# Performance work log

Hardware: AMD Instinct MI355X
Metric: run time of the kernel (lower is better)

Reference implementation:

```python
import jax, jax.numpy as jnp
import numpy as np

ALPHA = 0.2          # LeakyReLU negative slope
NEG = -9.0e15        # masking value from the torch code
B, N, F, O, H = 8, 1024, 256, 128, 8


def setup_inputs() -> dict:
    key = jax.random.key(0)
    ks = jax.random.split(key, 12)
    inputs = jax.random.normal(ks[0], (B, N, F), dtype=jnp.float32)
    adj = jax.random.randint(ks[1], (B, N, N), 0, 2, dtype=jnp.int32)
    mask = jnp.ones((B, N), dtype=jnp.float32)  # unused by forward, kept for signature fidelity
    s = 0.08
    # per-head GAT layers (stacked): W [H,F,O], attention vector a split into src/dst halves
    W_att = jax.random.normal(ks[2], (H, F, O), dtype=jnp.float32) * s
    a_src = jax.random.normal(ks[3], (H, O), dtype=jnp.float32) * s
    a_dst = jax.random.normal(ks[4], (H, O), dtype=jnp.float32) * s
    # output GAT layer: in = H*O, out = O
    W_out = jax.random.normal(ks[5], (H * O, O), dtype=jnp.float32) * s
    ao_src = jax.random.normal(ks[6], (O,), dtype=jnp.float32) * s
    ao_dst = jax.random.normal(ks[7], (O,), dtype=jnp.float32) * s
    # nn.Linear(H*O, O) and nn.Linear(O, O)
    lin_w = jax.random.normal(ks[8], (O, H * O), dtype=jnp.float32) * s
    lin_b = jax.random.normal(ks[9], (O,), dtype=jnp.float32) * s
    ln_w = jax.random.normal(ks[10], (O, O), dtype=jnp.float32) * s
    ln_b = jax.random.normal(ks[11], (O,), dtype=jnp.float32) * s
    return {"inputs": inputs, "adj": adj, "mask": mask, "W_att": W_att, "a_src": a_src,
            "a_dst": a_dst, "W_out": W_out, "ao_src": ao_src, "ao_dst": ao_dst,
            "lin_w": lin_w, "lin_b": lin_b, "ln_w": ln_w, "ln_b": ln_b}


def _gat_heads(x, adj, W, asrc, adst):
    # x: [B,N,Fin], W: [Hh,Fin,O]. e[b,h,i,j] = leakyrelu(h_i.a_src + h_j.a_dst)
    # (equal to torch's repeat/cat @ a without the O(N^2*2F) intermediate)
    h = jnp.einsum('bnf,hfo->bhno', x, W)
    s1 = jnp.einsum('bhno,ho->bhn', h, asrc)
    s2 = jnp.einsum('bhno,ho->bhn', h, adst)
    e = jax.nn.leaky_relu(s1[:, :, :, None] + s2[:, :, None, :], ALPHA)
    att = jax.nn.softmax(jnp.where(adj[:, None, :, :] > 0, e, NEG), axis=-1)
    return jnp.einsum('bhij,bhjo->bhio', att, h)  # [B,Hh,N,O]


def reference(inputs, adj, mask, W_att, a_src, a_dst, W_out, ao_src, ao_dst,
              lin_w, lin_b, ln_w, ln_b):
    b, n, _ = inputs.shape
    # layer 0: multi-head GAT, concat=True -> elu, then concat over heads
    hp = _gat_heads(inputs, adj, W_att, a_src, a_dst)              # [B,H,N,O]
    x = jax.nn.elu(hp).transpose(0, 2, 1, 3).reshape(b, n, -1)     # [B,N,H*O]
    # layer 1 (residual): linear(x) + out_att(x, adj) (concat=False, no elu)
    out = _gat_heads(x, adj, W_out[None], ao_src[None], ao_dst[None])[:, 0]  # [B,N,O]
    x = x @ lin_w.T + lin_b + out
    # final projection + relu
    return jax.nn.relu(x @ ln_w.T + ln_b)
```

## Files before the change

kernel.cpp:

```cpp
#include <hip/hip_runtime.h>


#define NN 1024
#define FF 256
#define OO 128
#define HH 8
#define HO 1024

typedef __attribute__((ext_vector_type(8))) short short8;
typedef __attribute__((ext_vector_type(4))) float floatx4;

__device__ __forceinline__ ushort f2b(float f) {
    union { float f; unsigned u; } v; v.f = f;
    unsigned r = v.u + 0x7FFFu + ((v.u >> 16) & 1u);
    return (ushort)(r >> 16);
}

__global__ __launch_bounds__(256) void pack_adj(
    const int* __restrict__ adj, unsigned long long* __restrict__ adjp)
{
    int w = blockIdx.x * 4 + (threadIdx.x >> 6);
    int lane = threadIdx.x & 63;
    const int* row = adj + (long)w * NN;
#pragma unroll
    for (int it = 0; it < 16; it++) {
        unsigned long long m = __ballot(row[it * 64 + lane] > 0);
        if (lane == 0) adjp[(long)w * 16 + it] = m;
    }
}

__global__ __launch_bounds__(256) void pack_weights(
    const float* __restrict__ W_att, const float* __restrict__ W_out,
    const float* __restrict__ lin_w, const float* __restrict__ ln_w,
    ushort* __restrict__ WAp, ushort* __restrict__ WOp,
    ushort* __restrict__ LWp, ushort* __restrict__ NWp)
{
    int tid = blockIdx.x * 256 + threadIdx.x;
    float v[8];
    ushort* dst;
    if (tid < 32768) {
        int h = tid >> 12, rem = tid & 4095, kc = rem >> 7, o = rem & 127;
        const float* s = W_att + h * 32768;
#pragma unroll
        for (int i = 0; i < 8; i++) v[i] = s[(kc * 8 + i) * 128 + o];
        dst = WAp + h * 32768 + kc * 1024 + o * 8;
    } else if (tid < 49152) {
        int t2 = tid - 32768;
        int kc = t2 >> 7, o = t2 & 127;
#pragma unroll
        for (int i = 0; i < 8; i++) v[i] = W_out[(kc * 8 + i) * 128 + o];
        dst = WOp + kc * 1024 + o * 8;
    } else if (tid < 65536) {
        int t3 = tid - 49152;
        int kc = t3 >> 7, c = t3 & 127;
        float4 a = *(const float4*)(lin_w + c * 1024 + kc * 8);
        float4 bq = *(const float4*)(lin_w + c * 1024 + kc * 8 + 4);
        v[0] = a.x; v[1] = a.y; v[2] = a.z; v[3] = a.w;
        v[4] = bq.x; v[5] = bq.y; v[6] = bq.z; v[7] = bq.w;
        dst = LWp + kc * 1024 + c * 8;
    } else {
        int t4 = tid - 65536;
        int kc = t4 >> 7, c = t4 & 127;
        float4 a = *(const float4*)(ln_w + c * 128 + kc * 8);
        float4 bq = *(const float4*)(ln_w + c * 128 + kc * 8 + 4);
        v[0] = a.x; v[1] = a.y; v[2] = a.z; v[3] = a.w;
        v[4] = bq.x; v[5] = bq.y; v[6] = bq.z; v[7] = bq.w;
        dst = NWp + kc * 1024 + c * 8;
    }
    union { ushort s[8]; uint4 q; } u;
#pragma unroll
    for (int i = 0; i < 8; i++) u.s[i] = f2b(v[i]);
    *(uint4*)dst = u.q;
}

__global__ __launch_bounds__(256) void gemmT0(
    const ushort* __restrict__ WAp, const float* __restrict__ inputs,
    ushort* __restrict__ Cb, float* __restrict__ s1, float* __restrict__ s2,
    const float* __restrict__ a1g, const float* __restrict__ a2g)
{
    __shared__ ushort Bs[32 * 520];
    int t = threadIdx.x;
    int wave = t >> 6, lane = t & 63;
    int quad = lane >> 4, l16 = lane & 15;
    int bh = blockIdx.y;
    int hh = bh & 7, b = bh >> 3;
    int nblk = blockIdx.x * 64;
    int n0w = nblk + wave * 16;

    const float* binp = inputs + ((long)b * NN + nblk) * FF;
#pragma unroll
    for (int it = 0; it < 8; it++) {
        int pid = it * 256 + t;
        int kc = pid & 31, r = pid >> 5;
        float4 va = *(const float4*)(binp + r * FF + kc * 8);
        float4 vb = *(const float4*)(binp + r * FF + kc * 8 + 4);
        union { ushort s[8]; uint4 q; } u;
        u.s[0] = f2b(va.x); u.s[1] = f2b(va.y); u.s[2] = f2b(va.z); u.s[3] = f2b(va.w);
        u.s[4] = f2b(vb.x); u.s[5] = f2b(vb.y); u.s[6] = f2b(vb.z); u.s[7] = f2b(vb.w);
        *(uint4*)&Bs[kc * 520 + r * 8] = u.q;
    }
    __syncthreads();

    const ushort* A = WAp + hh * 32768;
    int nl = wave * 16 + l16;
    floatx4 acc[8];
    floatx4 zero = {0.f, 0.f, 0.f, 0.f};
#pragma unroll
    for (int mt = 0; mt < 8; mt++) acc[mt] = zero;

#pragma unroll 2
    for (int kc2 = 0; kc2 < 8; kc2++) {
        int kc = kc2 * 4 + quad;
        short8 bfr = *(const short8*)&Bs[kc * 520 + nl * 8];
#pragma unroll
        for (int mt = 0; mt < 8; mt++) {
            short8 af = *(const short8*)(A + kc * 1024 + (mt * 16 + l16) * 8);
            acc[mt] = __builtin_amdgcn_mfma_f32_16x16x32_bf16(af, bfr, acc[mt], 0, 0, 0);
        }
    }

    const float* a1 = a1g + hh * OO;
    const float* a2 = a2g + hh * OO;
    float sp1 = 0.f, sp2 = 0.f;
#pragma unroll
    for (int mt = 0; mt < 8; mt++) {
        float4 v1 = *(const float4*)(a1 + mt * 16 + quad * 4);
        float4 v2 = *(const float4*)(a2 + mt * 16 + quad * 4);
        sp1 += acc[mt][0] * v1.x + acc[mt][1] * v1.y + acc[mt][2] * v1.z + acc[mt][3] * v1.w;
        sp2 += acc[mt][0] * v2.x + acc[mt][1] * v2.y + acc[mt][2] * v2.z + acc[mt][3] * v2.w;
    }
    sp1 += __shfl_xor(sp1, 16); sp1 += __shfl_xor(sp1, 32);
    sp2 += __shfl_xor(sp2, 16); sp2 += __shfl_xor(sp2, 32);
    if (lane < 16) {
        s1[(long)bh * NN + n0w + l16] = sp1;
        s2[(long)bh * NN + n0w + l16] = sp2;
    }

    ushort* cb = Cb + (long)bh * OO * NN;
    int n = n0w + l16;
    int base = (n >> 3) * 1024 + (n & 7);
#pragma unroll
    for (int mt = 0; mt < 8; mt++) {
#pragma unroll
        for (int reg = 0; reg < 4; reg++) {
            int o = mt * 16 + quad * 4 + reg;
            cb[base + o * 8] = f2b(acc[mt][reg]);
        }
    }
}

__global__ __launch_bounds__(256) void gemmT_sk(
    const ushort* __restrict__ WOp,
    const ushort* __restrict__ Bb,
    ushort* __restrict__ Cb,
    float* __restrict__ s1, float* __restrict__ s2,
    const float* __restrict__ a1g, const float* __restrict__ a2g)
{
    __shared__ float red[4 * 2304];
    int t = threadIdx.x;
    int wave = t >> 6, lane = t & 63;
    int quad = lane >> 4, l16 = lane & 15;
    int b = blockIdx.y;
    int n0 = blockIdx.x * 16;

    const ushort* brow = Bb + ((long)b * NN + n0 + l16) * HO;
    int kbase = wave * 256;

    floatx4 acc[8];
    floatx4 zero = {0.f, 0.f, 0.f, 0.f};
#pragma unroll
    for (int mt = 0; mt < 8; mt++) acc[mt] = zero;

    for (int k0 = 0; k0 < 256; k0 += 32) {
        int kb = kbase + k0 + quad * 8;
        int kch = kb >> 3;
        short8 bfr = *(const short8*)(brow + kb);
#pragma unroll
        for (int mt = 0; mt < 8; mt++) {
            short8 af = *(const short8*)(WOp + kch * 1024 + (mt * 16 + l16) * 8);
            acc[mt] = __builtin_amdgcn_mfma_f32_16x16x32_bf16(af, bfr, acc[mt], 0, 0, 0);
        }
    }

#pragma unroll
    for (int mt = 0; mt < 8; mt++)
#pragma unroll
        for (int reg = 0; reg < 4; reg++)
            red[wave * 2304 + (mt * 16 + quad * 4 + reg) * 18 + l16] = acc[mt][reg];
    __syncthreads();

    int nl = t & 15, g = t >> 4, o0 = g * 8;
    float s[8];
#pragma unroll
    for (int k = 0; k < 8; k++) {
        int idx = (o0 + k) * 18 + nl;
        s[k] = red[idx] + red[2304 + idx] + red[4608 + idx] + red[6912 + idx];
    }

    float p1 = 0.f, p2 = 0.f;
#pragma unroll
    for (int k = 0; k < 8; k++) {
        p1 += s[k] * a1g[o0 + k];
        p2 += s[k] * a2g[o0 + k];
    }

    ushort* cb = Cb + (long)b * OO * NN;
    int nglob = n0 + nl;
    int base = (nglob >> 3) * 1024 + (nglob & 7);
#pragma unroll
    for (int k = 0; k < 8; k++) cb[base + (o0 + k) * 8] = f2b(s[k]);

    __syncthreads();
    red[g * 16 + nl] = p1;
    red[256 + g * 16 + nl] = p2;
    __syncthreads();
    if (t < 16) {
        float q1 = 0.f, q2 = 0.f;
#pragma unroll
        for (int gg = 0; gg < 16; gg++) {
            q1 += red[gg * 16 + t];
            q2 += red[256 + gg * 16 + t];
        }
        s1[(long)b * NN + n0 + t] = q1;
        s2[(long)b * NN + n0 + t] = q2;
    }
}

template <int JS>
__global__ __launch_bounds__(256) void attn_mfma(
    const float* __restrict__ s1g, const float* __restrict__ s2g,
    const ushort* __restrict__ hTp, const uint* __restrict__ adjp,
    float* __restrict__ outf, ushort* __restrict__ outb,
    int Hh, int outStride, int doElu, int writeBf)
{
    extern __shared__ float smem_f[];
    float* s2s = smem_f;
    float* red = smem_f + NN;
    float* Lred = red + 8448;

    int t = threadIdx.x;
    int wave = t >> 6, lane = t & 63;
    int quad = lane >> 4, l16 = lane & 15;
    int bh = blockIdx.y;
    int hh = bh % Hh, b = bh / Hh;

    const float* s2r = s2g + (long)bh * NN;
    for (int j = t; j < NN; j += 256) s2s[j] = s2r[j];
    __syncthreads();

    const ushort* hT = hTp + (long)bh * OO * NN;
    const ushort* hbase = hT + quad * 1024 + l16 * 8;
    floatx4 zero = {0.f, 0.f, 0.f, 0.f};

    if (JS == 2) {
        int ig = wave >> 1, jh = wave & 1;
        int i0 = blockIdx.x * 64 + ig * 32;
        int j_lo = jh * (NN / 2), j_hi = j_lo + NN / 2;

        float s1a = s1g[(long)bh * NN + i0 + l16];
        float s1b = s1g[(long)bh * NN + i0 + 16 + l16];
        const uint* abA = adjp + ((long)b * NN + i0 + l16) * 32;
        const uint* abB = abA + 16 * 32;

        floatx4 acc0[8], acc1[8];
#pragma unroll
        for (int ot = 0; ot < 8; ot++) { acc0[ot] = zero; acc1[ot] = zero; }
        float Lp0 = 0.f, Lp1 = 0.f;

        for (int j0 = j_lo; j0 < j_hi; j0 += 32) {
            const ushort* hp = hbase + (j0 >> 3) * 1024;
            short8 bf[8];
#pragma unroll
            for (int ot = 0; ot < 8; ot++)
                bf[ot] = *(const short8*)(hp + ot * 128);
            uint mbA = (abA[j0 >> 5] >> (quad * 8)) & 0xffu;
            uint mbB = (abB[j0 >> 5] >> (quad * 8)) & 0xffu;
            int kb = j0 + quad * 8;
            float4 sA4 = *(const float4*)(s2s + kb);
            float4 sB4 = *(const float4*)(s2s + kb + 4);
            float se[8] = {sA4.x, sA4.y, sA4.z, sA4.w, sB4.x, sB4.y, sB4.z, sB4.w};
            short8 afA, afB;
#pragma unroll
            for (int e = 0; e < 8; e++) {
                float ea = s1a + se[e]; ea = fmaxf(ea, 0.2f * ea);
                float eb = s1b + se[e]; eb = fmaxf(eb, 0.2f * eb);
                union { float f; uint u; } wa, wb;
                wa.f = ((mbA >> e) & 1u) ? __expf(ea) : 0.f;
                wb.f = ((mbB >> e) & 1u) ? __expf(eb) : 0.f;
                wa.u &= 0xffff0000u; wb.u &= 0xffff0000u;
                afA[e] = (short)(wa.u >> 16);
                afB[e] = (short)(wb.u >> 16);
                Lp0 += wa.f; Lp1 += wb.f;
            }
#pragma unroll
            for (int ot = 0; ot < 8; ot++) {
                acc0[ot] = __builtin_amdgcn_mfma_f32_16x16x32_bf16(afA, bf[ot], acc0[ot], 0, 0, 0);
                acc1[ot] = __builtin_amdgcn_mfma_f32_16x16x32_bf16(afB, bf[ot], acc1[ot], 0, 0, 0);
            }
        }

        Lp0 += __shfl_xor(Lp0, 16); Lp0 += __shfl_xor(Lp0, 32);
        Lp1 += __shfl_xor(Lp1, 16); Lp1 += __shfl_xor(Lp1, 32);

        if (jh == 1) {
#pragma unroll
            for (int ot = 0; ot < 8; ot++)
#pragma unroll
                for (int reg = 0; reg < 4; reg++) {
                    red[(ig * 32 + quad * 4 + reg) * 132 + ot * 16 + l16] = acc0[ot][reg];
                    red[(ig * 32 + 16 + quad * 4 + reg) * 132 + ot * 16 + l16] = acc1[ot][reg];
                }
            if (lane < 16) {
                Lred[(ig * 2 + 0) * 16 + l16] = Lp0;
                Lred[(ig * 2 + 1) * 16 + l16] = Lp1;
            }
        }
        __syncthreads();
        if (jh == 0) {
            float r0 = 1.0f / (Lp0 + Lred[(ig * 2 + 0) * 16 + l16]);
            float r1 = 1.0f / (Lp1 + Lred[(ig * 2 + 1) * 16 + l16]);
#pragma unroll
            for (int tile = 0; tile < 2; tile++) {
                float rv = tile ? r1 : r0;
                floatx4* ac = tile ? acc1 : acc0;
#pragma unroll
                for (int reg = 0; reg < 4; reg++) {
                    float linv = __shfl(rv, quad * 4 + reg);
                    int rloc = ig * 32 + tile * 16 + quad * 4 + reg;
                    int row = blockIdx.x * 64 + rloc;
                    if (writeBf) {
                        ushort* orow = outb + (long)b * NN * outStride + hh * OO +
                                       (long)row * outStride + l16;
#pragma unroll
                        for (int ot = 0; ot < 8; ot++) {
                            float v = (ac[ot][reg] + red[rloc * 132 + ot * 16 + l16]) * linv;
                            if (doElu) v = (v > 0.f) ? v : (__expf(v) - 1.0f);
                            orow[ot * 16] = f2b(v);
                        }
                    } else {
                        float* orow = outf + (long)b * NN * outStride + hh * OO +
                                      (long)row * outStride + l16;
#pragma unroll
                        for (int ot = 0; ot < 8; ot++) {
                            float v = (ac[ot][reg] + red[rloc * 132 + ot * 16 + l16]) * linv;
                            if (doElu) v = (v > 0.f) ? v : (__expf(v) - 1.0f);
                            orow[ot * 16] = v;
                        }
                    }
                }
            }
        }
    } else {
        int i0 = blockIdx.x * 16;
        int j_lo = wave * (NN / 4), j_hi = j_lo + NN / 4;

        float s1a = s1g[(long)bh * NN + i0 + l16];
        const uint* abA = adjp + ((long)b * NN + i0 + l16) * 32;

        floatx4 acc[8];
#pragma unroll
        for (int ot = 0; ot < 8; ot++) acc[ot] = zero;
        float Lp = 0.f;

        for (int j0 = j_lo; j0 < j_hi; j0 += 32) {
            const ushort* hp = hbase + (j0 >> 3) * 1024;
            short8 bf[8];
#pragma unroll
            for (int ot = 0; ot < 8; ot++)
                bf[ot] = *(const short8*)(hp + ot * 128);
            uint mbA = (abA[j0 >> 5] >> (quad * 8)) & 0xffu;
            int kb = j0 + quad * 8;
            float4 sA4 = *(const float4*)(s2s + kb);
            float4 sB4 = *(const float4*)(s2s + kb + 4);
            float se[8] = {sA4.x, sA4.y, sA4.z, sA4.w, sB4.x, sB4.y, sB4.z, sB4.w};
            short8 afA;
#pragma unroll
            for (int e = 0; e < 8; e++) {
                float ea = s1a + se[e]; ea = fmaxf(ea, 0.2f * ea);
                union { float f; uint u; } wa;
                wa.f = ((mbA >> e) & 1u) ? __expf(ea) : 0.f;
                wa.u &= 0xffff0000u;
                afA[e] = (short)(wa.u >> 16);
                Lp += wa.f;
            }
#pragma unroll
            for (int ot = 0; ot < 8; ot++)
                acc[ot] = __builtin_amdgcn_mfma_f32_16x16x32_bf16(afA, bf[ot], acc[ot], 0, 0, 0);
        }

        Lp += __shfl_xor(Lp, 16); Lp += __shfl_xor(Lp, 32);
#pragma unroll
        for (int ot = 0; ot < 8; ot++)
#pragma unroll
            for (int reg = 0; reg < 4; reg++)
                red[(wave * 16 + quad * 4 + reg) * 132 + ot * 16 + l16] = acc[ot][reg];
        if (lane < 16) Lred[wave * 16 + l16] = Lp;
        __syncthreads();
        int row = t >> 4, c0 = (t & 15) * 8;
        float L = Lred[row] + Lred[16 + row] + Lred[32 + row] + Lred[48 + row];
        float rinv = 1.0f / L;
        int grow = i0 + row;
        float vv[8];
#pragma unroll
        for (int k = 0; k < 8; k++) {
            float s = red[row * 132 + c0 + k] + red[(16 + row) * 132 + c0 + k] +
                      red[(32 + row) * 132 + c0 + k] + red[(48 + row) * 132 + c0 + k];
            float v = s * rinv;
            if (doElu) v = (v > 0.f) ? v : (__expf(v) - 1.0f);
            vv[k] = v;
        }
        if (writeBf) {
            ushort* orow = outb + (long)b * NN * outStride + hh * OO +
                           (long)grow * outStride + c0;
#pragma unroll
            for (int k = 0; k < 8; k++) orow[k] = f2b(vv[k]);
        } else {
            float* orow = outf + (long)b * NN * outStride + hh * OO +
                          (long)grow * outStride + c0;
            *(float4*)orow = make_float4(vv[0], vv[1], vv[2], vv[3]);
            *(float4*)(orow + 4) = make_float4(vv[4], vv[5], vv[6], vv[7]);
        }
    }
}

__global__ __launch_bounds__(256) void final_mfma(
    const ushort* __restrict__ xb, const float* __restrict__ out2,
    const ushort* __restrict__ LWp, const float* __restrict__ lin_b,
    const ushort* __restrict__ NWp, const float* __restrict__ ln_b,
    float* __restrict__ out)
{
    __shared__ ushort ys[32][136];
    int t = threadIdx.x;
    int wave = t >> 6, lane = t & 63;
    int quad = lane >> 4, l16 = lane & 15;
    long row0 = (long)blockIdx.x * 32;
    int n0 = wave * 32;

    floatx4 zero = {0.f, 0.f, 0.f, 0.f};
    floatx4 acc[2][2];
#pragma unroll
    for (int mt = 0; mt < 2; mt++)
#pragma unroll
        for (int nt = 0; nt < 2; nt++) acc[mt][nt] = zero;

    for (int k0 = 0; k0 < HO; k0 += 32) {
        int kb = k0 + quad * 8;
        int kch = kb >> 3;
        short8 a0 = *(const short8*)(xb + (row0 + l16) * HO + kb);
        short8 a1 = *(const short8*)(xb + (row0 + 16 + l16) * HO + kb);
        short8 b0 = *(const short8*)(LWp + kch * 1024 + (n0 + l16) * 8);
        short8 b1 = *(const short8*)(LWp + kch * 1024 + (n0 + 16 + l16) * 8);
        acc[0][0] = __builtin_amdgcn_mfma_f32_16x16x32_bf16(a0, b0, acc[0][0], 0, 0, 0);
        acc[0][1] = __builtin_amdgcn_mfma_f32_16x16x32_bf16(a0, b1, acc[0][1], 0, 0, 0);
        acc[1][0] = __builtin_amdgcn_mfma_f32_16x16x32_bf16(a1, b0, acc[1][0], 0, 0, 0);
        acc[1][1] = __builtin_amdgcn_mfma_f32_16x16x32_bf16(a1, b1, acc[1][1], 0, 0, 0);
    }

#pragma unroll
    for (int nt = 0; nt < 2; nt++) {
        int col = n0 + nt * 16 + l16;
        float lb = lin_b[col];
#pragma unroll
        for (int mt = 0; mt < 2; mt++) {
#pragma unroll
            for (int reg = 0; reg < 4; reg++) {
                int row = mt * 16 + quad * 4 + reg;
                float v = acc[mt][nt][reg] + lb + out2[(row0 + row) * OO + col];
                ys[row][col] = f2b(v);
            }
        }
    }
    __syncthreads();

    floatx4 acc2[2][2];
#pragma unroll
    for (int mt = 0; mt < 2; mt++)
#pragma unroll
        for (int nt = 0; nt < 2; nt++) acc2[mt][nt] = zero;

#pragma unroll
    for (int k0 = 0; k0 < OO; k0 += 32) {
        int kb = k0 + quad * 8;
        int kch = kb >> 3;
        short8 a0 = *(const short8*)&ys[l16][kb];
        short8 a1 = *(const short8*)&ys[16 + l16][kb];
        short8 b0 = *(const short8*)(NWp + kch * 1024 + (n0 + l16) * 8);
        short8 b1 = *(const short8*)(NWp + kch * 1024 + (n0 + 16 + l16) * 8);
        acc2[0][0] = __builtin_amdgcn_mfma_f32_16x16x32_bf16(a0, b0, acc2[0][0], 0, 0, 0);
        acc2[0][1] = __builtin_amdgcn_mfma_f32_16x16x32_bf16(a0, b1, acc2[0][1], 0, 0, 0);
        acc2[1][0] = __builtin_amdgcn_mfma_f32_16x16x32_bf16(a1, b0, acc2[1][0], 0, 0, 0);
        acc2[1][1] = __builtin_amdgcn_mfma_f32_16x16x32_bf16(a1, b1, acc2[1][1], 0, 0, 0);
    }

#pragma unroll
    for (int nt = 0; nt < 2; nt++) {
        int col = n0 + nt * 16 + l16;
        float nb = ln_b[col];
#pragma unroll
        for (int mt = 0; mt < 2; mt++) {
#pragma unroll
            for (int reg = 0; reg < 4; reg++) {
                int row = mt * 16 + quad * 4 + reg;
                out[(row0 + row) * OO + col] = fmaxf(acc2[mt][nt][reg] + nb, 0.f);
            }
        }
    }
}

extern "C" void kernel_launch(void* const* d_in, const int* in_sizes, int n_in,
                              void* d_out, int out_size, void* d_ws, size_t ws_size,
                              hipStream_t stream)
{
    const float* inputs = (const float*)d_in[0];
    const int*   adj    = (const int*)d_in[1];
    const float* W_att  = (const float*)d_in[3];
    const float* a_src  = (const float*)d_in[4];
    const float* a_dst  = (const float*)d_in[5];
    const float* W_out  = (const float*)d_in[6];
    const float* ao_src = (const float*)d_in[7];
    const float* ao_dst = (const float*)d_in[8];
    const float* lin_w  = (const float*)d_in[9];
    const float* lin_b  = (const float*)d_in[10];
    const float* ln_w   = (const float*)d_in[11];
    const float* ln_b   = (const float*)d_in[12];
    float* out = (float*)d_out;

    float* ws   = (float*)d_ws;
    float* out2 = ws;
    float* s1   = ws + 1048576;
    float* s2   = ws + 1114112;
    float* s1o  = ws + 1179648;
    float* s2o  = ws + 1187840;
    ushort* ub      = (ushort*)(ws + 1196032);
    ushort* x_b     = ub;
    ushort* h_catTb = ub + 8388608;
    ushort* h2Tb    = ub + 16777216;
    ushort* WAp     = ub + 17825792;
    ushort* WOp     = ub + 18087936;
    ushort* LWp     = ub + 18219008;
    ushort* NWp     = ub + 18350080;
    unsigned long long* adjp = (unsigned long long*)(ub + 18366464);

    const int SH = (NN + 8448 + 64) * 4;

    pack_adj<<<2048, 256, 0, stream>>>(adj, adjp);
    pack_weights<<<264, 256, 0, stream>>>(
        W_att, W_out, lin_w, ln_w, WAp, WOp, LWp, NWp);
    gemmT0<<<dim3(16, 64), 256, 0, stream>>>(
        WAp, inputs, h_catTb, s1, s2, a_src, a_dst);
    attn_mfma<2><<<dim3(16, 64), 256, SH, stream>>>(
        s1, s2, h_catTb, (const uint*)adjp, (float*)nullptr, x_b, HH, HO, 1, 1);
    gemmT_sk<<<dim3(64, 8), 256, 0, stream>>>(
        WOp, x_b, h2Tb, s1o, s2o, ao_src, ao_dst);
    attn_mfma<4><<<dim3(64, 8), 256, SH, stream>>>(
        s1o, s2o, h2Tb, (const uint*)adjp, out2, (ushort*)nullptr, 1, OO, 0, 0);
    final_mfma<<<256, 256, 0, stream>>>(
        x_b, out2, LWp, lin_b, NWp, ln_b, out);
}
```

Before: 214.5 us.

## Merge pack kernels, compute softmax denominators via MFMA, use k-chunked x layout

After: 208.7 us. -2.7%, faster.

```diff
diff --git a/kernel.cpp b/kernel.cpp
--- a/kernel.cpp
+++ b/kernel.cpp
@@ -16,26 +16,25 @@
     return (ushort)(r >> 16);
 }
 
-__global__ __launch_bounds__(256) void pack_adj(
-    const int* __restrict__ adj, unsigned long long* __restrict__ adjp)
-{
-    int w = blockIdx.x * 4 + (threadIdx.x >> 6);
-    int lane = threadIdx.x & 63;
-    const int* row = adj + (long)w * NN;
-#pragma unroll
-    for (int it = 0; it < 16; it++) {
-        unsigned long long m = __ballot(row[it * 64 + lane] > 0);
-        if (lane == 0) adjp[(long)w * 16 + it] = m;
-    }
-}
-
-__global__ __launch_bounds__(256) void pack_weights(
+__global__ __launch_bounds__(256) void pack_all(
+    const int* __restrict__ adj, unsigned long long* __restrict__ adjp,
     const float* __restrict__ W_att, const float* __restrict__ W_out,
     const float* __restrict__ lin_w, const float* __restrict__ ln_w,
     ushort* __restrict__ WAp, ushort* __restrict__ WOp,
     ushort* __restrict__ LWp, ushort* __restrict__ NWp)
 {
-    int tid = blockIdx.x * 256 + threadIdx.x;
+    if (blockIdx.x < 2048) {
+        int w = blockIdx.x * 4 + (threadIdx.x >> 6);
+        int lane = threadIdx.x & 63;
+        const int* row = adj + (long)w * NN;
+#pragma unroll
+        for (int it = 0; it < 16; it++) {
+            unsigned long long m = __ballot(row[it * 64 + lane] > 0);
+            if (lane == 0) adjp[(long)w * 16 + it] = m;
+        }
+        return;
+    }
+    int tid = (blockIdx.x - 2048) * 256 + threadIdx.x;
     float v[8];
     ushort* dst;
     if (tid < 32768) {
@@ -150,10 +149,8 @@
 }
 
 __global__ __launch_bounds__(256) void gemmT_sk(
-    const ushort* __restrict__ WOp,
-    const ushort* __restrict__ Bb,
-    ushort* __restrict__ Cb,
-    float* __restrict__ s1, float* __restrict__ s2,
+    const ushort* __restrict__ WOp, const ushort* __restrict__ Bb,
+    ushort* __restrict__ Cb, float* __restrict__ s1, float* __restrict__ s2,
     const float* __restrict__ a1g, const float* __restrict__ a2g)
 {
     __shared__ float red[4 * 2304];
@@ -163,7 +160,7 @@
     int b = blockIdx.y;
     int n0 = blockIdx.x * 16;
 
-    const ushort* brow = Bb + ((long)b * NN + n0 + l16) * HO;
+    long rb = ((long)b * NN + n0 + l16) * 8;
     int kbase = wave * 256;
 
     floatx4 acc[8];
@@ -172,9 +169,8 @@
     for (int mt = 0; mt < 8; mt++) acc[mt] = zero;
 
     for (int k0 = 0; k0 < 256; k0 += 32) {
-        int kb = kbase + k0 + quad * 8;
-        int kch = kb >> 3;
-        short8 bfr = *(const short8*)(brow + kb);
+        int kch = (kbase + k0 + quad * 8) >> 3;
+        short8 bfr = *(const short8*)(Bb + (long)kch * 65536 + rb);
 #pragma unroll
         for (int mt = 0; mt < 8; mt++) {
             short8 af = *(const short8*)(WOp + kch * 1024 + (mt * 16 + l16) * 8);
@@ -251,6 +247,9 @@
     const ushort* hT = hTp + (long)bh * OO * NN;
     const ushort* hbase = hT + quad * 1024 + l16 * 8;
     floatx4 zero = {0.f, 0.f, 0.f, 0.f};
+    short8 ones8;
+#pragma unroll
+    for (int i = 0; i < 8; i++) ones8[i] = (short)0x3F80;
 
     if (JS == 2) {
         int ig = wave >> 1, jh = wave & 1;
@@ -262,10 +261,9 @@
         const uint* abA = adjp + ((long)b * NN + i0 + l16) * 32;
         const uint* abB = abA + 16 * 32;
 
-        floatx4 acc0[8], acc1[8];
+        floatx4 acc0[8], acc1[8], accL0 = zero, accL1 = zero;
 #pragma unroll
         for (int ot = 0; ot < 8; ot++) { acc0[ot] = zero; acc1[ot] = zero; }
-        float Lp0 = 0.f, Lp1 = 0.f;
 
         for (int j0 = j_lo; j0 < j_hi; j0 += 32) {
             const ushort* hp = hbase + (j0 >> 3) * 1024;
@@ -287,20 +285,17 @@
                 union { float f; uint u; } wa, wb;
                 wa.f = ((mbA >> e) & 1u) ? __expf(ea) : 0.f;
                 wb.f = ((mbB >> e) & 1u) ? __expf(eb) : 0.f;
-                wa.u &= 0xffff0000u; wb.u &= 0xffff0000u;
                 afA[e] = (short)(wa.u >> 16);
                 afB[e] = (short)(wb.u >> 16);
-                Lp0 += wa.f; Lp1 += wb.f;
             }
 #pragma unroll
             for (int ot = 0; ot < 8; ot++) {
                 acc0[ot] = __builtin_amdgcn_mfma_f32_16x16x32_bf16(afA, bf[ot], acc0[ot], 0, 0, 0);
                 acc1[ot] = __builtin_amdgcn_mfma_f32_16x16x32_bf16(afB, bf[ot], acc1[ot], 0, 0, 0);
             }
-        }
-
-        Lp0 += __shfl_xor(Lp0, 16); Lp0 += __shfl_xor(Lp0, 32);
-        Lp1 += __shfl_xor(Lp1, 16); Lp1 += __shfl_xor(Lp1, 32);
+            accL0 = __builtin_amdgcn_mfma_f32_16x16x32_bf16(afA, ones8, accL0, 0, 0, 0);
+            accL1 = __builtin_amdgcn_mfma_f32_16x16x32_bf16(afB, ones8, accL1, 0, 0, 0);
+        }
 
         if (jh == 1) {
 #pragma unroll
@@ -310,32 +305,34 @@
                     red[(ig * 32 + quad * 4 + reg) * 132 + ot * 16 + l16] = acc0[ot][reg];
                     red[(ig * 32 + 16 + quad * 4 + reg) * 132 + ot * 16 + l16] = acc1[ot][reg];
                 }
-            if (lane < 16) {
-                Lred[(ig * 2 + 0) * 16 + l16] = Lp0;
-                Lred[(ig * 2 + 1) * 16 + l16] = Lp1;
+            if (l16 == 0) {
+#pragma unroll
+                for (int reg = 0; reg < 4; reg++) {
+                    Lred[(ig * 2 + 0) * 16 + quad * 4 + reg] = accL0[reg];
+                    Lred[(ig * 2 + 1) * 16 + quad * 4 + reg] = accL1[reg];
+                }
             }
         }
         __syncthreads();
         if (jh == 0) {
-            float r0 = 1.0f / (Lp0 + Lred[(ig * 2 + 0) * 16 + l16]);
-            float r1 = 1.0f / (Lp1 + Lred[(ig * 2 + 1) * 16 + l16]);
 #pragma unroll
             for (int tile = 0; tile < 2; tile++) {
-                float rv = tile ? r1 : r0;
+                floatx4 acL = tile ? accL1 : accL0;
                 floatx4* ac = tile ? acc1 : acc0;
 #pragma unroll
                 for (int reg = 0; reg < 4; reg++) {
-                    float linv = __shfl(rv, quad * 4 + reg);
+                    float Lsum = acL[reg] + Lred[(ig * 2 + tile) * 16 + quad * 4 + reg];
+                    float linv = 1.0f / Lsum;
                     int rloc = ig * 32 + tile * 16 + quad * 4 + reg;
                     int row = blockIdx.x * 64 + rloc;
                     if (writeBf) {
-                        ushort* orow = outb + (long)b * NN * outStride + hh * OO +
-                                       (long)row * outStride + l16;
+                        long rg = (long)b * NN + row;
 #pragma unroll
                         for (int ot = 0; ot < 8; ot++) {
                             float v = (ac[ot][reg] + red[rloc * 132 + ot * 16 + l16]) * linv;
                             if (doElu) v = (v > 0.f) ? v : (__expf(v) - 1.0f);
-                            orow[ot * 16] = f2b(v);
+                            int col = hh * OO + ot * 16 + l16;
+                            outb[(long)(col >> 3) * 65536 + rg * 8 + (col & 7)] = f2b(v);
                         }
                     } else {
                         float* orow = outf + (long)b * NN * outStride + hh * OO +
@@ -357,10 +354,9 @@
         float s1a = s1g[(long)bh * NN + i0 + l16];
         const uint* abA = adjp + ((long)b * NN + i0 + l16) * 32;
 
-        floatx4 acc[8];
+        floatx4 acc[8], accL = zero;
 #pragma unroll
         for (int ot = 0; ot < 8; ot++) acc[ot] = zero;
-        float Lp = 0.f;
 
         for (int j0 = j_lo; j0 < j_hi; j0 += 32) {
             const ushort* hp = hbase + (j0 >> 3) * 1024;
@@ -379,22 +375,24 @@
                 float ea = s1a + se[e]; ea = fmaxf(ea, 0.2f * ea);
                 union { float f; uint u; } wa;
                 wa.f = ((mbA >> e) & 1u) ? __expf(ea) : 0.f;
-                wa.u &= 0xffff0000u;
                 afA[e] = (short)(wa.u >> 16);
-                Lp += wa.f;
             }
 #pragma unroll
             for (int ot = 0; ot < 8; ot++)
                 acc[ot] = __builtin_amdgcn_mfma_f32_16x16x32_bf16(afA, bf[ot], acc[ot], 0, 0, 0);
-        }
-
-        Lp += __shfl_xor(Lp, 16); Lp += __shfl_xor(Lp, 32);
+            accL = __builtin_amdgcn_mfma_f32_16x16x32_bf16(afA, ones8, accL, 0, 0, 0);
+        }
+
 #pragma unroll
         for (int ot = 0; ot < 8; ot++)
 #pragma unroll
             for (int reg = 0; reg < 4; reg++)
                 red[(wave * 16 + quad * 4 + reg) * 132 + ot * 16 + l16] = acc[ot][reg];
-        if (lane < 16) Lred[wave * 16 + l16] = Lp;
+        if (l16 == 0) {
+#pragma unroll
+            for (int reg = 0; reg < 4; reg++)
+                Lred[wave * 16 + quad * 4 + reg] = accL[reg];
+        }
         __syncthreads();
         int row = t >> 4, c0 = (t & 15) * 8;
         float L = Lred[row] + Lred[16 + row] + Lred[32 + row] + Lred[48 + row];
@@ -444,10 +442,9 @@
         for (int nt = 0; nt < 2; nt++) acc[mt][nt] = zero;
 
     for (int k0 = 0; k0 < HO; k0 += 32) {
-        int kb = k0 + quad * 8;
-        int kch = kb >> 3;
-        short8 a0 = *(const short8*)(xb + (row0 + l16) * HO + kb);
-        short8 a1 = *(const short8*)(xb + (row0 + 16 + l16) * HO + kb);
+        int kch = (k0 + quad * 8) >> 3;
+        short8 a0 = *(const short8*)(xb + (long)kch * 65536 + (row0 + l16) * 8);
+        short8 a1 = *(const short8*)(xb + (long)kch * 65536 + (row0 + 16 + l16) * 8);
         short8 b0 = *(const short8*)(LWp + kch * 1024 + (n0 + l16) * 8);
         short8 b1 = *(const short8*)(LWp + kch * 1024 + (n0 + 16 + l16) * 8);
         acc[0][0] = __builtin_amdgcn_mfma_f32_16x16x32_bf16(a0, b0, acc[0][0], 0, 0, 0);
@@ -543,9 +540,8 @@
 
     const int SH = (NN + 8448 + 64) * 4;
 
-    pack_adj<<<2048, 256, 0, stream>>>(adj, adjp);
-    pack_weights<<<264, 256, 0, stream>>>(
-        W_att, W_out, lin_w, ln_w, WAp, WOp, LWp, NWp);
+    pack_all<<<2312, 256, 0, stream>>>(
+        adj, adjp, W_att, W_out, lin_w, ln_w, WAp, WOp, LWp, NWp);
     gemmT0<<<dim3(16, 64), 256, 0, stream>>>(
         WAp, inputs, h_catTb, s1, s2, a_src, a_dst);
     attn_mfma<2><<<dim3(16, 64), 256, SH, stream>>>(
```
